# Kernel optimization log

Measured on AMD Instinct MI355X. Metric: run time of the kernel, lower is better.

## Reference

```python
import jax, jax.numpy as jnp
import numpy as np

N_REL = 32
N_ATTR = 8
WIDTH = 256
N_ENT = 2048


def setup_inputs() -> dict:
    key = jax.random.key(0)
    k1, k2, k3 = jax.random.split(key, 3)
    database = jax.random.uniform(k1, (N_REL, N_ENT, N_ENT), dtype=jnp.float32)
    attributes = jax.random.uniform(k2, (N_ATTR, N_ENT), dtype=jnp.float32)
    weights = jax.random.normal(k3, (2 * N_REL + N_ATTR, WIDTH), dtype=jnp.float32)
    return {"database": database, "attributes": attributes, "weights": weights}


def reference(database, attributes, weights):
    # per-relation reductions over each entity dim: [R, N] each
    q = jnp.concatenate([
        database.sum(axis=1),          # sum over dim 1 -> [R, N]
        database.sum(axis=2),          # sum over dim 2 -> [R, N]
        attributes * 2.0,              # [A, N]
    ], axis=0)                          # [2R + A, N]
    quantified = 1.0 - jnp.exp(-q)
    # softmax over rows of weights (axis 0), then [W, 2R+A] @ [2R+A, N]
    w = jax.nn.softmax(weights, axis=0)
    outputs = jnp.einsum('kw,kn->wn', w, quantified)  # [WIDTH, N]
    return outputs, quantified
```

## Files before the change

### kernel.cpp

```cpp
#include <hip/hip_runtime.h>
#include <math.h>

#define NREL  32
#define NENT  2048
#define NATTR 8
#define WIDTH 256
#define NK    (2 * NREL + NATTR)
#define CHUNKS_OUT 16
#define SUBS  4

typedef float f4 __attribute__((ext_vector_type(4)));

__global__ __launch_bounds__(256) void reduce_db_kernel(
    const float* __restrict__ db,
    float* __restrict__ qout,
    float* __restrict__ partial,
    int rowsPerWave,
    int nSubs)
{
    const int bx   = blockIdx.x;
    const int r    = bx >> 4;
    const int cOut = bx & (CHUNKS_OUT - 1);
    const int tid  = threadIdx.x;
    const int wave = tid >> 6;
    const int lane = tid & 63;

    __shared__ __align__(16) float smem[4][NENT];
    float (*rpart)[33] = reinterpret_cast<float(*)[33]>(&smem[0][0]);

    const size_t rowStride = NENT / 4;
    const f4* relBase = reinterpret_cast<const f4*>(db)
                      + (size_t)r * NENT * rowStride
                      + (size_t)(cOut * 128) * rowStride
                      + lane;

    f4 acc[8];
#pragma unroll
    for (int k = 0; k < 8; ++k) acc[k] = (f4)0.f;

    for (int sc = 0; sc < nSubs; ++sc) {
        const int i0 = sc * 32;
        const f4* base = relBase
                       + (size_t)(i0 + wave * rowsPerWave) * rowStride;

        for (int j = 0; j < rowsPerWave; j += 2) {
            const f4* rowA = base + (size_t)j * rowStride;
            const f4* rowB = rowA + rowStride;
            float rsA = 0.f, rsB = 0.f;
#pragma unroll
            for (int k = 0; k < 8; ++k) {
                f4 v = __builtin_nontemporal_load(rowA + k * 64);
                acc[k] += v;
                rsA += (v.x + v.y) + (v.z + v.w);
            }
#pragma unroll
            for (int k = 0; k < 8; ++k) {
                f4 v = __builtin_nontemporal_load(rowB + k * 64);
                acc[k] += v;
                rsB += (v.x + v.y) + (v.z + v.w);
            }
            rpart[lane][wave * rowsPerWave + j]     = rsA;
            rpart[lane][wave * rowsPerWave + j + 1] = rsB;
        }
        __syncthreads();

        {
            const int row = tid >> 3;
            const int seg = tid & 7;
            float t = 0.f;
#pragma unroll
            for (int i = 0; i < 8; ++i) t += rpart[seg * 8 + i][row];
            t += __shfl_xor(t, 1, 64);
            t += __shfl_xor(t, 2, 64);
            t += __shfl_xor(t, 4, 64);
            if (seg == 0)
                qout[(size_t)(NREL + r) * NENT + cOut * 128 + i0 + row] =
                    1.f - __expf(-t);
        }
        __syncthreads();
    }

#pragma unroll
    for (int k = 0; k < 8; ++k)
        *reinterpret_cast<f4*>(&smem[wave][k * 256 + lane * 4]) = acc[k];
    __syncthreads();

    f4* part4 = reinterpret_cast<f4*>(partial) + (size_t)bx * rowStride;
    for (int g = tid; g < NENT / 4; g += 256) {
        f4 a0 = *reinterpret_cast<const f4*>(&smem[0][g * 4]);
        f4 a1 = *reinterpret_cast<const f4*>(&smem[1][g * 4]);
        f4 a2 = *reinterpret_cast<const f4*>(&smem[2][g * 4]);
        f4 a3 = *reinterpret_cast<const f4*>(&smem[3][g * 4]);
        part4[g] = (a0 + a1) + (a2 + a3);
    }
}

#define MM_BLOCKS  (NENT / 64)
#define FIN_BLOCKS ((NREL + NATTR) * NENT / 256)

__global__ __launch_bounds__(256) void tail_kernel(
    const float* __restrict__ partial,
    const float* __restrict__ attrs,
    const float* __restrict__ W,
    float* __restrict__ qout,
    float* __restrict__ out)
{
    const int b   = blockIdx.x;
    const int tid = threadIdx.x;

    if (b < MM_BLOCKS) {
        __shared__ __align__(16) float qt[NK][68];
        const int c0  = b * 64;
        const int cq  = c0 >> 2;
        const f4* part4  = reinterpret_cast<const f4*>(partial);
        const f4* qout4  = reinterpret_cast<const f4*>(qout);
        const f4* attrs4 = reinterpret_cast<const f4*>(attrs);

        for (int s = tid; s < 32 * 16; s += 256) {
            const int row = s >> 4;
            const int cf  = s & 15;
            f4 sum = (f4)0.f;
#pragma unroll
            for (int c = 0; c < CHUNKS_OUT; ++c)
                sum += part4[(size_t)(row * CHUNKS_OUT + c) * 512 + cq + cf];
            f4 q;
            q.x = 1.f - __expf(-sum.x); q.y = 1.f - __expf(-sum.y);
            q.z = 1.f - __expf(-sum.z); q.w = 1.f - __expf(-sum.w);
            *reinterpret_cast<f4*>(&qt[row][cf * 4]) = q;
        }
        for (int s = tid; s < 32 * 16; s += 256) {
            const int row = s >> 4;
            const int cf  = s & 15;
            *reinterpret_cast<f4*>(&qt[32 + row][cf * 4]) =
                qout4[(size_t)(32 + row) * 512 + cq + cf];
        }
        if (tid < 8 * 16) {
            const int row = tid >> 4;
            const int cf  = tid & 15;
            f4 v = attrs4[(size_t)row * 512 + cq + cf];
            f4 q;
            q.x = 1.f - __expf(-2.f * v.x); q.y = 1.f - __expf(-2.f * v.y);
            q.z = 1.f - __expf(-2.f * v.z); q.w = 1.f - __expf(-2.f * v.w);
            *reinterpret_cast<f4*>(&qt[64 + row][cf * 4]) = q;
        }
        __syncthreads();

        const int w = tid;
        float m = W[w];
#pragma unroll
        for (int k = 1; k < NK; ++k) m = fmaxf(m, W[k * WIDTH + w]);
        float ssum = 0.f;
#pragma unroll
        for (int k = 0; k < NK; ++k) ssum += __expf(W[k * WIDTH + w] - m);
        const float inv = 1.f / ssum;

        f4 acc[16];
#pragma unroll
        for (int i = 0; i < 16; ++i) acc[i] = (f4)0.f;
        for (int k = 0; k < NK; ++k) {
            const float s = __expf(W[k * WIDTH + w] - m) * inv;
            const f4* qrow = reinterpret_cast<const f4*>(&qt[k][0]);
#pragma unroll
            for (int i = 0; i < 16; ++i) acc[i] += s * qrow[i];
        }
        f4* o4 = reinterpret_cast<f4*>(out + (size_t)w * NENT + c0);
#pragma unroll
        for (int i = 0; i < 16; ++i) o4[i] = acc[i];
    } else {
        const int idx = (b - MM_BLOCKS) * 256 + tid;
        const int row = idx >> 11;
        const int n   = idx & (NENT - 1);
        if (row < NREL) {
            float s = 0.f;
#pragma unroll
            for (int c = 0; c < CHUNKS_OUT; ++c)
                s += partial[((size_t)(row * CHUNKS_OUT + c) << 11) + n];
            qout[((size_t)row << 11) + n] = 1.f - __expf(-s);
        } else {
            const int a = row - NREL;
            float v = attrs[((size_t)a << 11) + n];
            qout[((size_t)(2 * NREL + a) << 11) + n] = 1.f - __expf(-2.f * v);
        }
    }
}

extern "C" void kernel_launch(void* const* d_in, const int* in_sizes, int n_in,
                              void* d_out, int out_size, void* d_ws, size_t ws_size,
                              hipStream_t stream)
{
    const float* db    = (const float*)d_in[0];
    const float* attrs = (const float*)d_in[1];
    const float* W     = (const float*)d_in[2];

    float* out   = (float*)d_out;
    float* quant = out + (size_t)WIDTH * NENT;

    float* partial = (float*)d_ws;

    reduce_db_kernel<<<NREL * CHUNKS_OUT, 256, 0, stream>>>(
        db, quant, partial, 8, SUBS);
    tail_kernel<<<MM_BLOCKS + FIN_BLOCKS, 256, 0, stream>>>(
        partial, attrs, W, quant, out);
}
```

Before: 116.8 us.

## Retile matmul tail into width x column blocks with shared softmax weights

```diff
diff --git a/kernel.cpp b/kernel.cpp
--- a/kernel.cpp
+++ b/kernel.cpp
@@ -95,7 +95,7 @@
     }
 }
 
-#define MM_BLOCKS  (NENT / 64)
+#define MM_BLOCKS  ((WIDTH / 32) * (NENT / 128))
 #define FIN_BLOCKS ((NREL + NATTR) * NENT / 256)
 
 __global__ __launch_bounds__(256) void tail_kernel(
@@ -109,63 +109,72 @@
     const int tid = threadIdx.x;
 
     if (b < MM_BLOCKS) {
-        __shared__ __align__(16) float qt[NK][68];
-        const int c0  = b * 64;
-        const int cq  = c0 >> 2;
+        __shared__ __align__(16) float qt[NK][132];
+        __shared__ float wsl[NK][33];
+        const int wg = b >> 4;
+        const int cg = b & 15;
+        const int w0 = wg * 32;
+        const int c0 = cg * 128;
+        const int cq = c0 >> 2;
+
         const f4* part4  = reinterpret_cast<const f4*>(partial);
         const f4* qout4  = reinterpret_cast<const f4*>(qout);
         const f4* attrs4 = reinterpret_cast<const f4*>(attrs);
 
-        for (int s = tid; s < 32 * 16; s += 256) {
-            const int row = s >> 4;
-            const int cf  = s & 15;
-            f4 sum = (f4)0.f;
-#pragma unroll
-            for (int c = 0; c < CHUNKS_OUT; ++c)
-                sum += part4[(size_t)(row * CHUNKS_OUT + c) * 512 + cq + cf];
+        for (int i = tid; i < NK * 32; i += 256) {
+            const int k  = i >> 5;
+            const int cf = i & 31;
             f4 q;
-            q.x = 1.f - __expf(-sum.x); q.y = 1.f - __expf(-sum.y);
-            q.z = 1.f - __expf(-sum.z); q.w = 1.f - __expf(-sum.w);
-            *reinterpret_cast<f4*>(&qt[row][cf * 4]) = q;
-        }
-        for (int s = tid; s < 32 * 16; s += 256) {
-            const int row = s >> 4;
-            const int cf  = s & 15;
-            *reinterpret_cast<f4*>(&qt[32 + row][cf * 4]) =
-                qout4[(size_t)(32 + row) * 512 + cq + cf];
-        }
-        if (tid < 8 * 16) {
-            const int row = tid >> 4;
-            const int cf  = tid & 15;
-            f4 v = attrs4[(size_t)row * 512 + cq + cf];
-            f4 q;
-            q.x = 1.f - __expf(-2.f * v.x); q.y = 1.f - __expf(-2.f * v.y);
-            q.z = 1.f - __expf(-2.f * v.z); q.w = 1.f - __expf(-2.f * v.w);
-            *reinterpret_cast<f4*>(&qt[64 + row][cf * 4]) = q;
-        }
-        __syncthreads();
-
-        const int w = tid;
-        float m = W[w];
-#pragma unroll
-        for (int k = 1; k < NK; ++k) m = fmaxf(m, W[k * WIDTH + w]);
-        float ssum = 0.f;
-#pragma unroll
-        for (int k = 0; k < NK; ++k) ssum += __expf(W[k * WIDTH + w] - m);
-        const float inv = 1.f / ssum;
-
-        f4 acc[16];
-#pragma unroll
-        for (int i = 0; i < 16; ++i) acc[i] = (f4)0.f;
+            if (k < NREL) {
+                f4 sum = (f4)0.f;
+#pragma unroll
+                for (int c = 0; c < CHUNKS_OUT; ++c)
+                    sum += part4[(size_t)(k * CHUNKS_OUT + c) * 512 + cq + cf];
+                q.x = 1.f - __expf(-sum.x); q.y = 1.f - __expf(-sum.y);
+                q.z = 1.f - __expf(-sum.z); q.w = 1.f - __expf(-sum.w);
+            } else if (k < 2 * NREL) {
+                q = qout4[(size_t)k * 512 + cq + cf];
+            } else {
+                f4 v = attrs4[(size_t)(k - 2 * NREL) * 512 + cq + cf];
+                q.x = 1.f - __expf(-2.f * v.x); q.y = 1.f - __expf(-2.f * v.y);
+                q.z = 1.f - __expf(-2.f * v.z); q.w = 1.f - __expf(-2.f * v.w);
+            }
+            *reinterpret_cast<f4*>(&qt[k][cf * 4]) = q;
+        }
+        for (int i = tid; i < NK * 32; i += 256) {
+            const int k  = i >> 5;
+            const int wl = i & 31;
+            wsl[k][wl] = W[k * WIDTH + w0 + wl];
+        }
+        __syncthreads();
+
+        if (tid < 32) {
+            const int wl = tid;
+            float m = wsl[0][wl];
+#pragma unroll
+            for (int k = 1; k < NK; ++k) m = fmaxf(m, wsl[k][wl]);
+            float s = 0.f;
+            float e[NK];
+#pragma unroll
+            for (int k = 0; k < NK; ++k) { e[k] = __expf(wsl[k][wl] - m); s += e[k]; }
+            const float inv = 1.f / s;
+#pragma unroll
+            for (int k = 0; k < NK; ++k) wsl[k][wl] = e[k] * inv;
+        }
+        __syncthreads();
+
+        const int wl = tid >> 3;
+        const int cl = (tid & 7) * 16;
+        f4 a0 = (f4)0.f, a1 = (f4)0.f, a2 = (f4)0.f, a3 = (f4)0.f;
+#pragma unroll 8
         for (int k = 0; k < NK; ++k) {
-            const float s = __expf(W[k * WIDTH + w] - m) * inv;
-            const f4* qrow = reinterpret_cast<const f4*>(&qt[k][0]);
-#pragma unroll
-            for (int i = 0; i < 16; ++i) acc[i] += s * qrow[i];
-        }
-        f4* o4 = reinterpret_cast<f4*>(out + (size_t)w * NENT + c0);
-#pragma unroll
-        for (int i = 0; i < 16; ++i) o4[i] = acc[i];
+            const float s = wsl[k][wl];
+            const f4* row = reinterpret_cast<const f4*>(&qt[k][cl]);
+            f4 v0 = row[0], v1 = row[1], v2 = row[2], v3 = row[3];
+            a0 += s * v0; a1 += s * v1; a2 += s * v2; a3 += s * v3;
+        }
+        f4* o4 = reinterpret_cast<f4*>(out + (size_t)(w0 + wl) * NENT + c0 + cl);
+        o4[0] = a0; o4[1] = a1; o4[2] = a2; o4[3] = a3;
     } else {
         const int idx = (b - MM_BLOCKS) * 256 + tid;
         const int row = idx >> 11;
```

Measured after the change: 100.6 us. -13.8%, faster.
